# Performance work log

Hardware: AMD Instinct MI355X
Metric: run time of the kernel (lower is better)

The kernel has to match this reference:

```python
import jax, jax.numpy as jnp
import numpy as np

ENC_DIM = 128
DEC_DIM = 128
NUM_HEADS = 4
HEAD_DIM = DEC_DIM // NUM_HEADS


def _layernorm(x, g, b, eps=1e-5):
    mu = jnp.mean(x, axis=-1, keepdims=True)
    var = jnp.mean((x - mu) ** 2, axis=-1, keepdims=True)
    return (x - mu) * jax.lax.rsqrt(var + eps) * g + b


def setup_inputs() -> dict:
    key = jax.random.key(0)
    ks = jax.random.split(key, 12)
    B, H, W, D = 2, 16, 16, 16
    s = 0.02
    return {
        "encoder_feat": jax.random.normal(ks[0], (B, ENC_DIM, H, W, D), jnp.float32),
        "decoder_feat": jax.random.normal(ks[1], (B, DEC_DIM, H, W, D), jnp.float32),
        # torch Linear weights stored as [out, in]
        "Wq": jax.random.normal(ks[2], (DEC_DIM, DEC_DIM), jnp.float32) * s,
        "bq": jnp.zeros((DEC_DIM,), jnp.float32),
        "Wk": jax.random.normal(ks[3], (DEC_DIM, ENC_DIM), jnp.float32) * s,
        "bk": jnp.zeros((DEC_DIM,), jnp.float32),
        "Wv": jax.random.normal(ks[4], (DEC_DIM, ENC_DIM), jnp.float32) * s,
        "bv": jnp.zeros((DEC_DIM,), jnp.float32),
        "Wo": jax.random.normal(ks[5], (DEC_DIM, DEC_DIM), jnp.float32) * s,
        "bo": jnp.zeros((DEC_DIM,), jnp.float32),
        "g_enc": jnp.ones((ENC_DIM,), jnp.float32),
        "b_enc": jnp.zeros((ENC_DIM,), jnp.float32),
        "g_dec": jnp.ones((DEC_DIM,), jnp.float32),
        "b_dec": jnp.zeros((DEC_DIM,), jnp.float32),
        "g_out": jnp.ones((DEC_DIM,), jnp.float32),
        "b_out": jnp.zeros((DEC_DIM,), jnp.float32),
        "W1": jax.random.normal(ks[6], (DEC_DIM * 4, DEC_DIM), jnp.float32) * s,
        "b1": jnp.zeros((DEC_DIM * 4,), jnp.float32),
        "W2": jax.random.normal(ks[7], (DEC_DIM, DEC_DIM * 4), jnp.float32) * s,
        "b2": jnp.zeros((DEC_DIM,), jnp.float32),
    }


def reference(encoder_feat, decoder_feat, Wq, bq, Wk, bk, Wv, bv, Wo, bo,
              g_enc, b_enc, g_dec, b_dec, g_out, b_out, W1, b1, W2, b2):
    B, C_dec, H, W_, D = decoder_feat.shape
    N = H * W_ * D
    scale = HEAD_DIM ** -0.5
    # [B, C, H, W, D] -> [B, N, C]
    enc_seq = encoder_feat.reshape(B, -1, N).transpose(0, 2, 1)
    dec_seq = decoder_feat.reshape(B, C_dec, N).transpose(0, 2, 1)
    enc_seq = _layernorm(enc_seq, g_enc, b_enc)
    dec_seq = _layernorm(dec_seq, g_dec, b_dec)
    # projections (torch Linear: x @ W.T + b), split heads -> [B, h, N, d]
    Q = (dec_seq @ Wq.T + bq).reshape(B, N, NUM_HEADS, HEAD_DIM).transpose(0, 2, 1, 3)
    K = (enc_seq @ Wk.T + bk).reshape(B, N, NUM_HEADS, HEAD_DIM).transpose(0, 2, 1, 3)
    V = (enc_seq @ Wv.T + bv).reshape(B, N, NUM_HEADS, HEAD_DIM).transpose(0, 2, 1, 3)
    attn = jnp.einsum('bhqd,bhkd->bhqk', Q, K) * scale  # [B, h, N, N]
    attn = jax.nn.softmax(attn, axis=-1)
    out = jnp.einsum('bhqk,bhkd->bhqd', attn, V)
    out = out.transpose(0, 2, 1, 3).reshape(B, N, C_dec)
    out = out @ Wo.T + bo
    out = dec_seq + out
    h = _layernorm(out, g_out, b_out)
    ffn = jax.nn.gelu(h @ W1.T + b1, approximate=False) @ W2.T + b2
    out = out + ffn
    return out.transpose(0, 2, 1).reshape(B, C_dec, H, W_, D)
```

## Files before the change

### kernel.cpp

```cpp
#include <hip/hip_runtime.h>
#include <hip/hip_bf16.h>
#include <math.h>

#define B_ 2
#define N_ 4096
#define BN_ 8192
#define NH_ 4
#define SPLIT_ 8

using bf16x8   = __attribute__((ext_vector_type(8))) __bf16;
using f32x4    = __attribute__((ext_vector_type(4))) float;
using ushortx8 = __attribute__((ext_vector_type(8))) unsigned short;

#if __has_builtin(__builtin_amdgcn_exp2f)
#define FAST_EXP2(x) __builtin_amdgcn_exp2f(x)
#else
#define FAST_EXP2(x) __expf((x) * 0.6931471805599453f)
#endif

static __device__ __forceinline__ unsigned short f2bf(float f) {
    union { __hip_bfloat16 h; unsigned short u; } c;
    c.h = __float2bfloat16(f);
    return c.u;
}
static __device__ __forceinline__ float bf2f(unsigned short u) {
    union { __hip_bfloat16 h; unsigned short u; } c;
    c.u = u;
    return __bfloat162float(c.h);
}
static __device__ __forceinline__ unsigned int pk2bf(float lo, float hi) {
    return __builtin_amdgcn_perm(__float_as_uint(hi) + 0x8000u,
                                 __float_as_uint(lo) + 0x8000u, 0x07060302u);
}

__global__ __launch_bounds__(256)
void convert_weights_kernel(const float* __restrict__ Wq, const float* __restrict__ Wk,
                            const float* __restrict__ Wv, const float* __restrict__ Wo,
                            const float* __restrict__ W1, const float* __restrict__ W2,
                            unsigned short* __restrict__ wq, unsigned short* __restrict__ wk,
                            unsigned short* __restrict__ wv, unsigned short* __restrict__ wo,
                            unsigned short* __restrict__ w1, unsigned short* __restrict__ w2) {
    const int id = blockIdx.x * 256 + threadIdx.x;
    if      (id <  16384) wq[id]          = f2bf(Wq[id]);
    else if (id <  32768) wk[id - 16384]  = f2bf(Wk[id - 16384]);
    else if (id <  49152) wv[id - 32768]  = f2bf(Wv[id - 32768]);
    else if (id <  65536) wo[id - 49152]  = f2bf(Wo[id - 49152]);
    else if (id < 131072) w1[id - 65536]  = f2bf(W1[id - 65536]);
    else                  w2[id - 131072] = f2bf(W2[id - 131072]);
}

__global__ __launch_bounds__(256)
void qkv2_kernel(const float* __restrict__ enc, const float* __restrict__ dec,
                 const float* __restrict__ g_enc, const float* __restrict__ b_enc,
                 const float* __restrict__ g_dec, const float* __restrict__ b_dec,
                 const unsigned short* __restrict__ wq,
                 const unsigned short* __restrict__ wk,
                 const unsigned short* __restrict__ wv,
                 const float* __restrict__ bq, const float* __restrict__ bk,
                 const float* __restrict__ bv,
                 unsigned short* __restrict__ Qh, unsigned short* __restrict__ Kh,
                 unsigned short* __restrict__ Vt,
                 unsigned short* __restrict__ dec_lnb) {
    __shared__ float tile[128][33];
    __shared__ float mu_s[32], inv_s[32];
    const int z  = blockIdx.y;
    const int t  = threadIdx.x;
    const int m0 = blockIdx.x * 32;
    const int b  = m0 >> 12, n0 = m0 & 4095;
    const float* inb   = ((z == 0) ? dec : enc) + (size_t)b * 128 * N_;
    const float* gamma = (z == 0) ? g_dec : g_enc;
    const float* beta  = (z == 0) ? b_dec : b_enc;

    {
        const int col = t & 31;
        const int r0  = t >> 5;
        #pragma unroll
        for (int j = 0; j < 16; ++j) {
            const int r = r0 + 8 * j;
            tile[r][col] = inb[(size_t)r * N_ + n0 + col];
        }
    }
    __syncthreads();
    {
        const int tok = t >> 3;
        const int ln  = t & 7;
        float s = 0.f, ss = 0.f;
        for (int c = ln; c < 128; c += 8) {
            const float x = tile[c][tok];
            s += x; ss += x * x;
        }
        for (int m = 1; m < 8; m <<= 1) {
            s  += __shfl_xor(s, m);
            ss += __shfl_xor(ss, m);
        }
        if (ln == 0) {
            const float mu  = s * (1.f / 128.f);
            mu_s[tok]  = mu;
            inv_s[tok] = rsqrtf(ss * (1.f / 128.f) - mu * mu + 1e-5f);
        }
    }
    __syncthreads();

    const int wvx = t >> 6, lane = t & 63;
    const int l15 = lane & 15, quad = lane >> 4;
    const int tokgrp  = (wvx & 1) * 16;
    const int colbase = (z == 0) ? (wvx >> 1) * 64 : 0;
    const bool isV    = (z == 1) && (wvx >> 1);
    const bool wrLN   = (z == 0) && ((wvx >> 1) == 0);
    const int nbCount = (z == 0) ? 4 : 8;
    const int tok = tokgrp + l15;
    const float mu  = mu_s[tok];
    const float inv = inv_s[tok];

    bf16x8 af[4];
    #pragma unroll
    for (int kk = 0; kk < 4; ++kk) {
        float y[8];
        #pragma unroll
        for (int j = 0; j < 8; ++j) {
            const int c = kk * 32 + quad * 8 + j;
            y[j] = (tile[c][tok] - mu) * inv * gamma[c] + beta[c];
        }
        union { uint4 u; bf16x8 v8; ushortx8 us; } cvt;
        cvt.u.x = pk2bf(y[0], y[1]); cvt.u.y = pk2bf(y[2], y[3]);
        cvt.u.z = pk2bf(y[4], y[5]); cvt.u.w = pk2bf(y[6], y[7]);
        af[kk] = cvt.v8;
        if (wrLN)
            *(ushortx8*)(dec_lnb + (size_t)(m0 + tok) * 128 + kk * 32 + quad * 8) = cvt.us;
    }

    const unsigned short* Wb = (z == 0) ? wq : (isV ? wv : wk);
    const float* bias        = (z == 0) ? bq : (isV ? bv : bk);
    const float sc = (z == 0) ? (0.17677669529663687f * 1.4426950408889634f) : 1.f;
    const int nbase = n0 + tokgrp + quad * 4;

    #pragma unroll
    for (int nb = 0; nb < 8; ++nb) {
        if (nb >= nbCount) break;
        const int col = colbase + nb * 16 + l15;
        f32x4 a = {0.f, 0.f, 0.f, 0.f};
        #pragma unroll
        for (int kk = 0; kk < 4; ++kk) {
            const bf16x8 wf = *(const bf16x8*)(Wb + (size_t)col * 128 + kk * 32 + quad * 8);
            a = __builtin_amdgcn_mfma_f32_16x16x32_bf16(af[kk], wf, a, 0, 0, 0);
        }
        const int h = col >> 5, d = col & 31;
        const float bz = bias[col];
        if (isV) {
            ushort4 pk;
            pk.x = f2bf(a[0] + bz);
            pk.y = f2bf(a[1] + bz);
            pk.z = f2bf(a[2] + bz);
            pk.w = f2bf(a[3] + bz);
            *(ushort4*)(Vt + ((size_t)(b * NH_ + h) * 32 + d) * N_ + nbase) = pk;
        } else {
            unsigned short* dst = (z == 0) ? Qh : Kh;
            #pragma unroll
            for (int r = 0; r < 4; ++r)
                dst[((size_t)(b * NH_ + h) * N_ + nbase + r) * 32 + d] = f2bf((a[r] + bz) * sc);
        }
    }
}

__global__ __launch_bounds__(256)
void attn_kernel5(const unsigned short* __restrict__ Qh,
                  const unsigned short* __restrict__ Kh,
                  const unsigned short* __restrict__ Vt,
                  unsigned short* __restrict__ Op,
                  unsigned short* __restrict__ lp) {
    __shared__ alignas(16) unsigned short sP[4][64][72];

    const int gid   = blockIdx.x;
    const int combo = gid & 63;
    const int qblk  = gid >> 6;
    const int bh    = combo & 7;
    const int s     = combo >> 3;
    const int t  = threadIdx.x;
    const int wvx = t >> 6, lane = t & 63;
    const int l15 = lane & 15, quad = lane >> 4;
    const int qw = qblk * 256 + wvx * 64;
    const size_t hbse = (size_t)bh * N_ * 32;

    bf16x8 qf[4];
    #pragma unroll
    for (int f = 0; f < 4; ++f)
        qf[f] = *(const bf16x8*)(Qh + hbse + (size_t)(qw + f * 16 + l15) * 32 + quad * 8);

    const unsigned short* Kp = Kh + hbse;
    const unsigned short* Vp = Vt + (size_t)bh * 32 * N_;

    f32x4 o0[4], o1[4];
    float l[4];
    #pragma unroll
    for (int f = 0; f < 4; ++f) {
        o0[f] = f32x4{0.f, 0.f, 0.f, 0.f};
        o1[f] = f32x4{0.f, 0.f, 0.f, 0.f};
        l[f] = 0.f;
    }
    const f32x4 zero = {0.f, 0.f, 0.f, 0.f};

    const int kbeg = s * (N_ / SPLIT_);
    const int kend = kbeg + (N_ / SPLIT_);

    bf16x8 kf[4];
    #pragma unroll
    for (int c = 0; c < 4; ++c)
        kf[c] = *(const bf16x8*)(Kp + (size_t)(kbeg + c * 16 + l15) * 32 + quad * 8);

    for (int k0 = kbeg; k0 < kend; k0 += 64) {
        bf16x8 va[2], vb[2];
        #pragma unroll
        for (int s2 = 0; s2 < 2; ++s2) {
            va[s2] = *(const bf16x8*)(Vp + (size_t)l15 * N_        + k0 + s2 * 32 + quad * 8);
            vb[s2] = *(const bf16x8*)(Vp + (size_t)(16 + l15) * N_ + k0 + s2 * 32 + quad * 8);
        }
        const int kn = (k0 + 64 < kend) ? (k0 + 64) : kbeg;
        bf16x8 kfn[4];
        #pragma unroll
        for (int c = 0; c < 4; ++c)
            kfn[c] = *(const bf16x8*)(Kp + (size_t)(kn + c * 16 + l15) * 32 + quad * 8);

        #pragma unroll
        for (int f = 0; f < 4; ++f) {
            #pragma unroll
            for (int c = 0; c < 4; ++c) {
                const f32x4 sv = __builtin_amdgcn_mfma_f32_16x16x32_bf16(kf[c], qf[f], zero, 0, 0, 0);
                const float p0 = FAST_EXP2(sv[0]);
                const float p1 = FAST_EXP2(sv[1]);
                const float p2 = FAST_EXP2(sv[2]);
                const float p3 = FAST_EXP2(sv[3]);
                l[f] += (p0 + p1) + (p2 + p3);
                uint2 pk;
                pk.x = pk2bf(p0, p1);
                pk.y = pk2bf(p2, p3);
                *(uint2*)&sP[wvx][f * 16 + l15][c * 16 + quad * 4] = pk;
            }
        }
        #pragma unroll
        for (int f = 0; f < 4; ++f) {
            #pragma unroll
            for (int s2 = 0; s2 < 2; ++s2) {
                const bf16x8 pf = *(const bf16x8*)&sP[wvx][f * 16 + l15][s2 * 32 + quad * 8];
                o0[f] = __builtin_amdgcn_mfma_f32_16x16x32_bf16(va[s2], pf, o0[f], 0, 0, 0);
                o1[f] = __builtin_amdgcn_mfma_f32_16x16x32_bf16(vb[s2], pf, o1[f], 0, 0, 0);
            }
        }
        #pragma unroll
        for (int c = 0; c < 4; ++c) kf[c] = kfn[c];
    }

    #pragma unroll
    for (int f = 0; f < 4; ++f) {
        float lf = l[f];
        lf += __shfl_xor(lf, 16);
        lf += __shfl_xor(lf, 32);
        const int tok = qw + f * 16 + l15;
        const size_t ob = ((size_t)(s * 8 + bh) * N_ + tok) * 32;
        uint2 w0, w1v;
        w0.x  = pk2bf(o0[f][0], o0[f][1]); w0.y  = pk2bf(o0[f][2], o0[f][3]);
        w1v.x = pk2bf(o1[f][0], o1[f][1]); w1v.y = pk2bf(o1[f][2], o1[f][3]);
        *(uint2*)&Op[ob + quad * 4]      = w0;
        *(uint2*)&Op[ob + 16 + quad * 4] = w1v;
        if (quad == 0)
            lp[(size_t)(s * 8 + bh) * N_ + tok] = f2bf(lf);
    }
}

__global__ __launch_bounds__(256)
void fused_tail3_kernel(const unsigned short* __restrict__ Op,
                        const unsigned short* __restrict__ lp,
                        const unsigned short* __restrict__ wo,
                        const float* __restrict__ bo,
                        const unsigned short* __restrict__ decb,
                        const float* __restrict__ g, const float* __restrict__ be,
                        const unsigned short* __restrict__ w1,
                        const float* __restrict__ b1,
                        const unsigned short* __restrict__ w2,
                        const float* __restrict__ b2,
                        float* __restrict__ out) {
    __shared__ alignas(16) unsigned short sredb[4][64][36];
    __shared__ float sln[4][2][16];
    __shared__ alignas(16) unsigned short hb_lds[16][136];
    __shared__ alignas(16) unsigned short smid[16][536];
    const int t = threadIdx.x;
    const int wv = t >> 6, lane = t & 63;
    const int l15 = lane & 15, quad = lane >> 4;
    const int m0 = blockIdx.x * 16;

    const int tokA = m0 + l15;
    const int bA = tokA >> 12, nA = tokA & 4095;
    const int bhh = bA * NH_ + wv;
    bf16x8 af;
    {
        f32x4 sa = {0.f, 0.f, 0.f, 0.f}, sb = {0.f, 0.f, 0.f, 0.f};
        float lt = 0.f;
        #pragma unroll
        for (int s = 0; s < SPLIT_; ++s) {
            const size_t base = ((size_t)(s * 8 + bhh) * N_ + nA) * 32 + quad * 8;
            const ushortx8 u = *(const ushortx8*)&Op[base];
            sa[0] += bf2f(u[0]); sa[1] += bf2f(u[1]);
            sa[2] += bf2f(u[2]); sa[3] += bf2f(u[3]);
            sb[0] += bf2f(u[4]); sb[1] += bf2f(u[5]);
            sb[2] += bf2f(u[6]); sb[3] += bf2f(u[7]);
            lt += bf2f(lp[(size_t)(s * 8 + bhh) * N_ + nA]);
        }
        const float inv = 1.f / lt;
        union { uint4 u; bf16x8 v; } cvt;
        cvt.u.x = pk2bf(sa[0] * inv, sa[1] * inv);
        cvt.u.y = pk2bf(sa[2] * inv, sa[3] * inv);
        cvt.u.z = pk2bf(sb[0] * inv, sb[1] * inv);
        cvt.u.w = pk2bf(sb[2] * inv, sb[3] * inv);
        af = cvt.v;
    }

    #pragma unroll
    for (int nb = 0; nb < 8; ++nb) {
        const bf16x8 wf = *(const bf16x8*)(wo + (size_t)(nb * 16 + l15) * 128
                                           + wv * 32 + quad * 8);
        const f32x4 a = __builtin_amdgcn_mfma_f32_16x16x32_bf16(
            af, wf, f32x4{0.f, 0.f, 0.f, 0.f}, 0, 0, 0);
        uint2 p;
        p.x = pk2bf(a[0], a[1]);
        p.y = pk2bf(a[2], a[3]);
        *(uint2*)&sredb[wv][lane][nb * 4] = p;
    }
    __syncthreads();

    float v[2][4];
    #pragma unroll
    for (int lnb = 0; lnb < 2; ++lnb) {
        const int nbg = 2 * wv + lnb;
        f32x4 p = {0.f, 0.f, 0.f, 0.f};
        #pragma unroll
        for (int w = 0; w < 4; ++w) {
            const ushort4 u = *(const ushort4*)&sredb[w][lane][nbg * 4];
            p[0] += bf2f(u.x); p[1] += bf2f(u.y);
            p[2] += bf2f(u.z); p[3] += bf2f(u.w);
        }
        const int col = nbg * 16 + l15;
        const float bz = bo[col];
        #pragma unroll
        for (int r = 0; r < 4; ++r) {
            const int tok = m0 + quad * 4 + r;
            v[lnb][r] = p[r] + bz + bf2f(decb[(size_t)tok * 128 + col]);
        }
    }

    {
        float s[4], ss[4];
        #pragma unroll
        for (int r = 0; r < 4; ++r) {
            float a = v[0][r] + v[1][r];
            float b = v[0][r] * v[0][r] + v[1][r] * v[1][r];
            for (int m = 1; m < 16; m <<= 1) {
                a += __shfl_xor(a, m);
                b += __shfl_xor(b, m);
            }
            s[r] = a; ss[r] = b;
        }
        if (l15 == 0) {
            #pragma unroll
            for (int r = 0; r < 4; ++r) {
                sln[wv][0][quad * 4 + r] = s[r];
                sln[wv][1][quad * 4 + r] = ss[r];
            }
        }
    }
    __syncthreads();

    {
        #pragma unroll
        for (int r = 0; r < 4; ++r) {
            const int tk = quad * 4 + r;
            const float stot  = sln[0][0][tk] + sln[1][0][tk] + sln[2][0][tk] + sln[3][0][tk];
            const float sstot = sln[0][1][tk] + sln[1][1][tk] + sln[2][1][tk] + sln[3][1][tk];
            const float mu  = stot * (1.f / 128.f);
            const float inv = rsqrtf(sstot * (1.f / 128.f) - mu * mu + 1e-5f);
            #pragma unroll
            for (int lnb = 0; lnb < 2; ++lnb) {
                const int col = (2 * wv + lnb) * 16 + l15;
                hb_lds[tk][col] = f2bf((v[lnb][r] - mu) * inv * g[col] + be[col]);
            }
        }
    }
    __syncthreads();

    bf16x8 hf[4];
    #pragma unroll
    for (int kk = 0; kk < 4; ++kk)
        hf[kk] = *(const bf16x8*)&hb_lds[l15][kk * 32 + quad * 8];
    #pragma unroll
    for (int nb = 0; nb < 8; ++nb) {
        const int col = wv * 128 + nb * 16 + l15;
        f32x4 a = {0.f, 0.f, 0.f, 0.f};
        #pragma unroll
        for (int kk = 0; kk < 4; ++kk) {
            const bf16x8 wf = *(const bf16x8*)(w1 + (size_t)col * 128 + kk * 32 + quad * 8);
            a = __builtin_amdgcn_mfma_f32_16x16x32_bf16(hf[kk], wf, a, 0, 0, 0);
        }
        const float bz = b1[col];
        #pragma unroll
        for (int r = 0; r < 4; ++r) {
            float x = a[r] + bz;
            x = 0.5f * x * (1.f + erff(x * 0.70710678118f));
            smid[quad * 4 + r][col] = f2bf(x);
        }
    }
    __syncthreads();

    f32x4 acc[8];
    #pragma unroll
    for (int nb = 0; nb < 8; ++nb) acc[nb] = f32x4{0.f, 0.f, 0.f, 0.f};
    #pragma unroll
    for (int kk = 0; kk < 4; ++kk) {
        const bf16x8 af2 = *(const bf16x8*)&smid[l15][wv * 128 + kk * 32 + quad * 8];
        #pragma unroll
        for (int nb = 0; nb < 8; ++nb) {
            const bf16x8 wf = *(const bf16x8*)(w2 + (size_t)(nb * 16 + l15) * 512
                                               + wv * 128 + kk * 32 + quad * 8);
            acc[nb] = __builtin_amdgcn_mfma_f32_16x16x32_bf16(af2, wf, acc[nb], 0, 0, 0);
        }
    }
    __syncthreads();
    #pragma unroll
    for (int nb = 0; nb < 8; ++nb) {
        uint2 p;
        p.x = pk2bf(acc[nb][0], acc[nb][1]);
        p.y = pk2bf(acc[nb][2], acc[nb][3]);
        *(uint2*)&sredb[wv][lane][nb * 4] = p;
    }
    __syncthreads();

    {
        const int b = m0 >> 12;
        const int nb0 = (m0 & 4095) + quad * 4;
        #pragma unroll
        for (int lnb = 0; lnb < 2; ++lnb) {
            const int nbg = 2 * wv + lnb;
            f32x4 p = {0.f, 0.f, 0.f, 0.f};
            #pragma unroll
            for (int w = 0; w < 4; ++w) {
                const ushort4 u = *(const ushort4*)&sredb[w][lane][nbg * 4];
                p[0] += bf2f(u.x); p[1] += bf2f(u.y);
                p[2] += bf2f(u.z); p[3] += bf2f(u.w);
            }
            const int col = nbg * 16 + l15;
            const float bz = b2[col];
            f32x4 res;
            #pragma unroll
            for (int r = 0; r < 4; ++r)
                res[r] = p[r] + bz + v[lnb][r];
            *(f32x4*)&out[((size_t)(b * 128 + col)) * N_ + nb0] = res;
        }
    }
}

extern "C" void kernel_launch(void* const* d_in, const int* in_sizes, int n_in,
                              void* d_out, int out_size, void* d_ws, size_t ws_size,
                              hipStream_t stream) {
    const float* enc   = (const float*)d_in[0];
    const float* dec   = (const float*)d_in[1];
    const float* Wq    = (const float*)d_in[2];
    const float* bq    = (const float*)d_in[3];
    const float* Wk    = (const float*)d_in[4];
    const float* bk    = (const float*)d_in[5];
    const float* Wv    = (const float*)d_in[6];
    const float* bv    = (const float*)d_in[7];
    const float* Wo    = (const float*)d_in[8];
    const float* bo    = (const float*)d_in[9];
    const float* g_enc = (const float*)d_in[10];
    const float* b_enc = (const float*)d_in[11];
    const float* g_dec = (const float*)d_in[12];
    const float* b_dec = (const float*)d_in[13];
    const float* g_out = (const float*)d_in[14];
    const float* b_out = (const float*)d_in[15];
    const float* W1    = (const float*)d_in[16];
    const float* b1    = (const float*)d_in[17];
    const float* W2    = (const float*)d_in[18];
    const float* b2    = (const float*)d_in[19];
    float* out = (float*)d_out;
    char*  W   = (char*)d_ws;

    unsigned short* wqb = (unsigned short*)(W);
    unsigned short* wkb = wqb + 16384;
    unsigned short* wvb = wkb + 16384;
    unsigned short* wob = wvb + 16384;
    unsigned short* w1b = wob + 16384;
    unsigned short* w2b = w1b + 65536;
    unsigned short* dec_lnb = (unsigned short*)(W + (2560ull << 10));
    unsigned short* Qh      = (unsigned short*)(W + (4608ull << 10));
    unsigned short* Kh      = (unsigned short*)(W + (6656ull << 10));
    unsigned short* Vt      = (unsigned short*)(W + (8704ull << 10));
    unsigned short* Op      = (unsigned short*)(W + (10752ull << 10));
    unsigned short* lpb     = (unsigned short*)(W + (27136ull << 10));

    convert_weights_kernel<<<768, 256, 0, stream>>>(Wq, Wk, Wv, Wo, W1, W2,
                                                    wqb, wkb, wvb, wob, w1b, w2b);

    qkv2_kernel<<<dim3(BN_ / 32, 2), 256, 0, stream>>>(
        enc, dec, g_enc, b_enc, g_dec, b_dec, wqb, wkb, wvb,
        bq, bk, bv, Qh, Kh, Vt, dec_lnb);

    attn_kernel5<<<1024, 256, 0, stream>>>(Qh, Kh, Vt, Op, lpb);

    fused_tail3_kernel<<<512, 256, 0, stream>>>(Op, lpb, wob, bo, dec_lnb,
                                                g_out, b_out, w1b, b1, w2b, b2, out);
}
```

Measured before the change: 167.6 us.

## Fold weight conversion into QKV kernel and merge attention splits in-block

Drops the separate weight-conversion launch. The QKV kernel now converts Wq/Wk/Wv from fp32 on the fly, and 72 extra blocks in the same launch convert Wo/W1/W2. The attention kernel runs 8 waves per block, each wave handling one KV split for the same 64 queries. The splits are reduced through LDS in fp32 and a normalized context is written directly, so the split partial outputs and denominators no longer make a bf16 round trip through global memory before the tail kernel. In exchange, attention blocks are larger (512 threads, more LDS), and the QKV weights are re-read and reconverted in every block.

```diff
diff --git a/kernel.cpp b/kernel.cpp
--- a/kernel.cpp
+++ b/kernel.cpp
@@ -32,40 +32,49 @@
     return __builtin_amdgcn_perm(__float_as_uint(hi) + 0x8000u,
                                  __float_as_uint(lo) + 0x8000u, 0x07060302u);
 }
+static __device__ __forceinline__ bf16x8 ldw(const float* __restrict__ W, size_t off) {
+    const float4 a = *(const float4*)(W + off);
+    const float4 b = *(const float4*)(W + off + 4);
+    union { uint4 u; bf16x8 v; } c;
+    c.u.x = pk2bf(a.x, a.y); c.u.y = pk2bf(a.z, a.w);
+    c.u.z = pk2bf(b.x, b.y); c.u.w = pk2bf(b.z, b.w);
+    return c.v;
+}
 
 __global__ __launch_bounds__(256)
-void convert_weights_kernel(const float* __restrict__ Wq, const float* __restrict__ Wk,
-                            const float* __restrict__ Wv, const float* __restrict__ Wo,
-                            const float* __restrict__ W1, const float* __restrict__ W2,
-                            unsigned short* __restrict__ wq, unsigned short* __restrict__ wk,
-                            unsigned short* __restrict__ wv, unsigned short* __restrict__ wo,
-                            unsigned short* __restrict__ w1, unsigned short* __restrict__ w2) {
-    const int id = blockIdx.x * 256 + threadIdx.x;
-    if      (id <  16384) wq[id]          = f2bf(Wq[id]);
-    else if (id <  32768) wk[id - 16384]  = f2bf(Wk[id - 16384]);
-    else if (id <  49152) wv[id - 32768]  = f2bf(Wv[id - 32768]);
-    else if (id <  65536) wo[id - 49152]  = f2bf(Wo[id - 49152]);
-    else if (id < 131072) w1[id - 65536]  = f2bf(W1[id - 65536]);
-    else                  w2[id - 131072] = f2bf(W2[id - 131072]);
-}
-
-__global__ __launch_bounds__(256)
-void qkv2_kernel(const float* __restrict__ enc, const float* __restrict__ dec,
+void qkv3_kernel(const float* __restrict__ enc, const float* __restrict__ dec,
                  const float* __restrict__ g_enc, const float* __restrict__ b_enc,
                  const float* __restrict__ g_dec, const float* __restrict__ b_dec,
-                 const unsigned short* __restrict__ wq,
-                 const unsigned short* __restrict__ wk,
-                 const unsigned short* __restrict__ wv,
+                 const float* __restrict__ Wq, const float* __restrict__ Wk,
+                 const float* __restrict__ Wv,
                  const float* __restrict__ bq, const float* __restrict__ bk,
                  const float* __restrict__ bv,
+                 const float* __restrict__ Wo, const float* __restrict__ W1,
+                 const float* __restrict__ W2,
+                 unsigned short* __restrict__ wo, unsigned short* __restrict__ w1,
+                 unsigned short* __restrict__ w2,
                  unsigned short* __restrict__ Qh, unsigned short* __restrict__ Kh,
                  unsigned short* __restrict__ Vt,
                  unsigned short* __restrict__ dec_lnb) {
+    const int t = threadIdx.x;
+    if (blockIdx.x >= 512) {
+        const int e = ((int)blockIdx.x - 512) * 256 * 8 + t * 8;
+        const float* src; unsigned short* dst; int off;
+        if (e < 16384)       { src = Wo; dst = wo; off = e; }
+        else if (e < 81920)  { src = W1; dst = w1; off = e - 16384; }
+        else                 { src = W2; dst = w2; off = e - 81920; }
+        const float4 a = *(const float4*)(src + off);
+        const float4 b = *(const float4*)(src + off + 4);
+        uint4 p;
+        p.x = pk2bf(a.x, a.y); p.y = pk2bf(a.z, a.w);
+        p.z = pk2bf(b.x, b.y); p.w = pk2bf(b.z, b.w);
+        *(uint4*)(dst + off) = p;
+        return;
+    }
     __shared__ float tile[128][33];
     __shared__ float mu_s[32], inv_s[32];
-    const int z  = blockIdx.y;
-    const int t  = threadIdx.x;
-    const int m0 = blockIdx.x * 32;
+    const int z  = blockIdx.x >> 8;
+    const int m0 = (blockIdx.x & 255) * 32;
     const int b  = m0 >> 12, n0 = m0 & 4095;
     const float* inb   = ((z == 0) ? dec : enc) + (size_t)b * 128 * N_;
     const float* gamma = (z == 0) ? g_dec : g_enc;
@@ -129,8 +138,8 @@
             *(ushortx8*)(dec_lnb + (size_t)(m0 + tok) * 128 + kk * 32 + quad * 8) = cvt.us;
     }
 
-    const unsigned short* Wb = (z == 0) ? wq : (isV ? wv : wk);
-    const float* bias        = (z == 0) ? bq : (isV ? bv : bk);
+    const float* Wb   = (z == 0) ? Wq : (isV ? Wv : Wk);
+    const float* bias = (z == 0) ? bq : (isV ? bv : bk);
     const float sc = (z == 0) ? (0.17677669529663687f * 1.4426950408889634f) : 1.f;
     const int nbase = n0 + tokgrp + quad * 4;
 
@@ -141,7 +150,7 @@
         f32x4 a = {0.f, 0.f, 0.f, 0.f};
         #pragma unroll
         for (int kk = 0; kk < 4; ++kk) {
-            const bf16x8 wf = *(const bf16x8*)(Wb + (size_t)col * 128 + kk * 32 + quad * 8);
+            const bf16x8 wf = ldw(Wb, (size_t)col * 128 + kk * 32 + quad * 8);
             a = __builtin_amdgcn_mfma_f32_16x16x32_bf16(af[kk], wf, a, 0, 0, 0);
         }
         const int h = col >> 5, d = col & 31;
@@ -162,23 +171,22 @@
     }
 }
 
-__global__ __launch_bounds__(256)
-void attn_kernel5(const unsigned short* __restrict__ Qh,
+__global__ __launch_bounds__(512)
+void attn_kernel7(const unsigned short* __restrict__ Qh,
                   const unsigned short* __restrict__ Kh,
                   const unsigned short* __restrict__ Vt,
-                  unsigned short* __restrict__ Op,
-                  unsigned short* __restrict__ lp) {
-    __shared__ alignas(16) unsigned short sP[4][64][72];
-
-    const int gid   = blockIdx.x;
-    const int combo = gid & 63;
-    const int qblk  = gid >> 6;
-    const int bh    = combo & 7;
-    const int s     = combo >> 3;
+                  unsigned short* __restrict__ ctx) {
+    __shared__ alignas(16) unsigned short sP[8][64][72];
+    __shared__ float ldsL[8][64];
+
+    const int gid  = blockIdx.x;
+    const int bh   = gid & 7;
+    const int qblk = gid >> 3;
     const int t  = threadIdx.x;
     const int wvx = t >> 6, lane = t & 63;
     const int l15 = lane & 15, quad = lane >> 4;
-    const int qw = qblk * 256 + wvx * 64;
+    const int s = wvx;
+    const int qw = qblk * 64;
     const size_t hbse = (size_t)bh * N_ * 32;
 
     bf16x8 qf[4];
@@ -249,26 +257,46 @@
         for (int c = 0; c < 4; ++c) kf[c] = kfn[c];
     }
 
+    float lf4[4];
     #pragma unroll
     for (int f = 0; f < 4; ++f) {
         float lf = l[f];
         lf += __shfl_xor(lf, 16);
         lf += __shfl_xor(lf, 32);
-        const int tok = qw + f * 16 + l15;
-        const size_t ob = ((size_t)(s * 8 + bh) * N_ + tok) * 32;
-        uint2 w0, w1v;
-        w0.x  = pk2bf(o0[f][0], o0[f][1]); w0.y  = pk2bf(o0[f][2], o0[f][3]);
-        w1v.x = pk2bf(o1[f][0], o1[f][1]); w1v.y = pk2bf(o1[f][2], o1[f][3]);
-        *(uint2*)&Op[ob + quad * 4]      = w0;
-        *(uint2*)&Op[ob + 16 + quad * 4] = w1v;
-        if (quad == 0)
-            lp[(size_t)(s * 8 + bh) * N_ + tok] = f2bf(lf);
-    }
+        lf4[f] = lf;
+    }
+
+    __syncthreads();
+    float* ldsO = (float*)&sP[0][0][0];
+    #pragma unroll
+    for (int f = 0; f < 4; ++f) {
+        const int q = f * 16 + l15;
+        float* row = ldsO + ((size_t)s * 64 + q) * 36;
+        *(f32x4*)(row + quad * 4)      = o0[f];
+        *(f32x4*)(row + 16 + quad * 4) = o1[f];
+        if (quad == 0) ldsL[s][q] = lf4[f];
+    }
+    __syncthreads();
+
+    const int tok = t >> 3;
+    const int d0  = (t & 7) * 4;
+    f32x4 sum = {0.f, 0.f, 0.f, 0.f};
+    float lsum = 0.f;
+    #pragma unroll
+    for (int w = 0; w < 8; ++w) {
+        sum  += *(const f32x4*)(ldsO + ((size_t)w * 64 + tok) * 36 + d0);
+        lsum += ldsL[w][tok];
+    }
+    const float inv = 1.f / lsum;
+    uint2 pk;
+    pk.x = pk2bf(sum[0] * inv, sum[1] * inv);
+    pk.y = pk2bf(sum[2] * inv, sum[3] * inv);
+    const int b = bh >> 2, h = bh & 3;
+    *(uint2*)(ctx + ((size_t)(b * N_ + qw + tok)) * 128 + h * 32 + d0) = pk;
 }
 
 __global__ __launch_bounds__(256)
-void fused_tail3_kernel(const unsigned short* __restrict__ Op,
-                        const unsigned short* __restrict__ lp,
+void fused_tail4_kernel(const unsigned short* __restrict__ ctx,
                         const unsigned short* __restrict__ wo,
                         const float* __restrict__ bo,
                         const unsigned short* __restrict__ decb,
@@ -288,30 +316,7 @@
     const int m0 = blockIdx.x * 16;
 
     const int tokA = m0 + l15;
-    const int bA = tokA >> 12, nA = tokA & 4095;
-    const int bhh = bA * NH_ + wv;
-    bf16x8 af;
-    {
-        f32x4 sa = {0.f, 0.f, 0.f, 0.f}, sb = {0.f, 0.f, 0.f, 0.f};
-        float lt = 0.f;
-        #pragma unroll
-        for (int s = 0; s < SPLIT_; ++s) {
-            const size_t base = ((size_t)(s * 8 + bhh) * N_ + nA) * 32 + quad * 8;
-            const ushortx8 u = *(const ushortx8*)&Op[base];
-            sa[0] += bf2f(u[0]); sa[1] += bf2f(u[1]);
-            sa[2] += bf2f(u[2]); sa[3] += bf2f(u[3]);
-            sb[0] += bf2f(u[4]); sb[1] += bf2f(u[5]);
-            sb[2] += bf2f(u[6]); sb[3] += bf2f(u[7]);
-            lt += bf2f(lp[(size_t)(s * 8 + bhh) * N_ + nA]);
-        }
-        const float inv = 1.f / lt;
-        union { uint4 u; bf16x8 v; } cvt;
-        cvt.u.x = pk2bf(sa[0] * inv, sa[1] * inv);
-        cvt.u.y = pk2bf(sa[2] * inv, sa[3] * inv);
-        cvt.u.z = pk2bf(sb[0] * inv, sb[1] * inv);
-        cvt.u.w = pk2bf(sb[2] * inv, sb[3] * inv);
-        af = cvt.v;
-    }
+    const bf16x8 af = *(const bf16x8*)(ctx + (size_t)tokA * 128 + wv * 32 + quad * 8);
 
     #pragma unroll
     for (int nb = 0; nb < 8; ++nb) {
@@ -481,28 +486,21 @@
     float* out = (float*)d_out;
     char*  W   = (char*)d_ws;
 
-    unsigned short* wqb = (unsigned short*)(W);
-    unsigned short* wkb = wqb + 16384;
-    unsigned short* wvb = wkb + 16384;
-    unsigned short* wob = wvb + 16384;
+    unsigned short* wob = (unsigned short*)(W);
     unsigned short* w1b = wob + 16384;
     unsigned short* w2b = w1b + 65536;
     unsigned short* dec_lnb = (unsigned short*)(W + (2560ull << 10));
     unsigned short* Qh      = (unsigned short*)(W + (4608ull << 10));
     unsigned short* Kh      = (unsigned short*)(W + (6656ull << 10));
     unsigned short* Vt      = (unsigned short*)(W + (8704ull << 10));
-    unsigned short* Op      = (unsigned short*)(W + (10752ull << 10));
-    unsigned short* lpb     = (unsigned short*)(W + (27136ull << 10));
-
-    convert_weights_kernel<<<768, 256, 0, stream>>>(Wq, Wk, Wv, Wo, W1, W2,
-                                                    wqb, wkb, wvb, wob, w1b, w2b);
-
-    qkv2_kernel<<<dim3(BN_ / 32, 2), 256, 0, stream>>>(
-        enc, dec, g_enc, b_enc, g_dec, b_dec, wqb, wkb, wvb,
-        bq, bk, bv, Qh, Kh, Vt, dec_lnb);
-
-    attn_kernel5<<<1024, 256, 0, stream>>>(Qh, Kh, Vt, Op, lpb);
-
-    fused_tail3_kernel<<<512, 256, 0, stream>>>(Op, lpb, wob, bo, dec_lnb,
+    unsigned short* ctx     = (unsigned short*)(W + (10752ull << 10));
+
+    qkv3_kernel<<<512 + 72, 256, 0, stream>>>(
+        enc, dec, g_enc, b_enc, g_dec, b_dec, Wq, Wk, Wv, bq, bk, bv,
+        Wo, W1, W2, wob, w1b, w2b, Qh, Kh, Vt, dec_lnb);
+
+    attn_kernel7<<<512, 512, 0, stream>>>(Qh, Kh, Vt, ctx);
+
+    fused_tail4_kernel<<<512, 256, 0, stream>>>(ctx, wob, bo, dec_lnb,
                                                 g_out, b_out, w1b, b1, w2b, b2, out);
 }
```

Result: no change. 166.0 us (-1.0%).
